# Performance work log

Hardware: AMD Instinct MI355X
Metric: run time of the kernel (lower is better)

Reference implementation:

```python
import jax, jax.numpy as jnp
import numpy as np

HIDDEN = 1024


def setup_inputs() -> dict:
    key = jax.random.key(0)
    ks = jax.random.split(key, 8)
    B, S, H = 64, 2048, HIDDEN
    scale = 1.0 / np.sqrt(H)
    return {
        "decoder_hidden": jax.random.normal(ks[0], (B, H), jnp.float32),
        "encoder_outputs": jax.random.normal(ks[1], (B, S, 2 * H), jnp.float32),
        "coverage": jax.random.uniform(ks[2], (B, S), jnp.float32),
        "mask": jnp.ones((B, S), jnp.int32),
        # parameters (nn.Linear weight layout: (out, in); we store transposed for x @ W)
        "W_h": jax.random.normal(ks[3], (2 * H, H), jnp.float32) * scale,
        "W_d": jax.random.normal(ks[4], (H, H), jnp.float32) * scale,
        "W_c": jax.random.normal(ks[5], (1, H), jnp.float32) * scale,
        "v": jax.random.normal(ks[6], (H, 1), jnp.float32) * scale,
    }


def reference(decoder_hidden, encoder_outputs, coverage, mask, W_h, W_d, W_c, v):
    # energy: (B, S, H) = tanh(enc@W_h + dec@W_d broadcast over S + coverage*W_c)
    enc_proj = jnp.einsum("bse,eh->bsh", encoder_outputs, W_h)
    dec_proj = (decoder_hidden @ W_d)[:, None, :]            # (B,1,H)
    cov_proj = coverage[:, :, None] * W_c[0][None, None, :]  # (B,S,H)
    energy = jnp.tanh(enc_proj + dec_proj + cov_proj)
    scores = jnp.einsum("bsh,h->bs", energy, v[:, 0])        # (B,S)
    scores = jnp.where(mask == 0, jnp.float32(-10000.0), scores)
    attn_weights = jax.nn.softmax(scores, axis=1)            # (B,S)
    coverage_new = coverage + attn_weights
    context = jnp.einsum("bs,bse->be", attn_weights, encoder_outputs)  # (B,2H)
    return (context, attn_weights, coverage_new)
```

## Files before the change

kernel.cpp:

```cpp
#include <hip/hip_runtime.h>
#include <hip/hip_bf16.h>
#include <stdint.h>

#define BATCH 64
#define SEQ   2048
#define HID   1024
#define EDIM  2048

#define BM 64
#define BK 32
#define KSTEPS (EDIM / BK)
#define SMEM_BYTES 141568

typedef __bf16 bf16x8 __attribute__((ext_vector_type(8)));
typedef float  f32x4  __attribute__((ext_vector_type(4)));

__device__ __forceinline__ unsigned short f2bf(float x) {
    __hip_bfloat16 h = __float2bfloat16(x);
    return __builtin_bit_cast(unsigned short, h);
}

__device__ __forceinline__ uint4 pack8(float4 f0, float4 f1) {
    uint4 r;
    r.x = (unsigned)f2bf(f0.x) | ((unsigned)f2bf(f0.y) << 16);
    r.y = (unsigned)f2bf(f0.z) | ((unsigned)f2bf(f0.w) << 16);
    r.z = (unsigned)f2bf(f1.x) | ((unsigned)f2bf(f1.y) << 16);
    r.w = (unsigned)f2bf(f1.z) | ((unsigned)f2bf(f1.w) << 16);
    return r;
}

__device__ __forceinline__ void gload16(const void* g, void* l) {
    __builtin_amdgcn_global_load_lds(
        (const __attribute__((address_space(1))) void*)g,
        (__attribute__((address_space(3))) void*)l, 16, 0, 0);
}

__global__ void wh_transpose_kernel(const float* __restrict__ Wh,
                                    unsigned short* __restrict__ Wt) {
    __shared__ float tile[32][33];
    int bx = blockIdx.x & 63;
    int by = blockIdx.x >> 6;
    int e0 = bx * 32, h0 = by * 32;
    int tx = threadIdx.x & 31, ty = threadIdx.x >> 5;
    #pragma unroll
    for (int i = 0; i < 4; ++i)
        tile[ty + 8 * i][tx] = Wh[(size_t)(e0 + ty + 8 * i) * HID + h0 + tx];
    __syncthreads();
    if (ty < 4) {
        uint4 wv;
        unsigned short* ws = (unsigned short*)&wv;
        #pragma unroll
        for (int j = 0; j < 8; ++j) ws[j] = f2bf(tile[ty * 8 + j][tx]);
        *(uint4*)&Wt[((size_t)(e0 >> 3) + ty) * 8192 + (size_t)(h0 + tx) * 8] = wv;
    }
}

__global__ void dec_proj_kernel(const float* __restrict__ dec,
                                const float* __restrict__ Wd,
                                float* __restrict__ dp) {
    int gid = blockIdx.x * 256 + threadIdx.x;
    int b = gid >> 10, h = gid & 1023;
    const float* dr = dec + b * HID;
    float acc = 0.f;
    #pragma unroll 4
    for (int k = 0; k < HID; ++k) acc = fmaf(dr[k], Wd[(size_t)k * HID + h], acc);
    dp[gid] = acc;
}

__global__ __launch_bounds__(1024, 4) void scores_kernel(
    const float* __restrict__ enc, const float* __restrict__ cov,
    const unsigned short* __restrict__ Wt, const float* __restrict__ dp,
    const float* __restrict__ Wc, const float* __restrict__ vv,
    float* __restrict__ scores)
{
    extern __shared__ char smem[];
    unsigned short* Blbase = (unsigned short*)smem;
    unsigned short* Albase = (unsigned short*)(smem + 131072);
    float* cov_s = (float*)(smem + 139264);
    float* sred  = (float*)(smem + 139520);

    const int tid  = threadIdx.x;
    const int lane = tid & 63;
    const int wid  = tid >> 6;
    const int wm   = wid >> 3;
    const int wn   = wid & 7;
    const int c15  = lane & 15;
    const int g    = lane >> 4;
    const int rsl  = (c15 & 3) ^ ((c15 >> 2) & 3);

    const int b  = blockIdx.x >> 5;
    const int s0 = (blockIdx.x & 31) * BM;

    const float* Abase = enc + (size_t)(b * SEQ + s0) * EDIM;

    const int arow = tid >> 2;
    const int ag   = tid & 3;
    const int asl  = ag ^ ((arow & 3) ^ ((arow >> 2) & 3));

    f32x4 acc[2][8];
    #pragma unroll
    for (int mi = 0; mi < 2; ++mi)
        #pragma unroll
        for (int nj = 0; nj < 8; ++nj)
            #pragma unroll
            for (int r = 0; r < 4; ++r) acc[mi][nj][r] = 0.f;

    if (tid < BM) cov_s[tid] = cov[b * SEQ + s0 + tid];

    {
        const unsigned short* bsrc = Wt + (size_t)tid * 8;
        unsigned short* bdst = Blbase + tid * 8;
        #pragma unroll
        for (int j = 0; j < 4; ++j)
            gload16(bsrc + (size_t)j * 8192, bdst + j * 8192);
        if (tid < 256) {
            const float* ap = Abase + (size_t)arow * EDIM + ag * 8;
            *(uint4*)(Albase + arow * 32 + asl * 8) =
                pack8(*(const float4*)ap, *(const float4*)(ap + 4));
        }
    }
    __syncthreads();

    float4 a0n, a1n;
    for (int kk = 0; kk < KSTEPS; ++kk) {
        const int cur = kk & 1, nxt = cur ^ 1;
        const unsigned short* Bcur = Blbase + cur * 32768;
        const unsigned short* Acur = Albase + cur * 2048;

        if (kk + 1 < KSTEPS) {
            const unsigned short* bsrc = Wt + (size_t)(kk + 1) * 32768 + (size_t)tid * 8;
            unsigned short* bdst = Blbase + nxt * 32768 + tid * 8;
            #pragma unroll
            for (int j = 0; j < 4; ++j)
                gload16(bsrc + (size_t)j * 8192, bdst + j * 8192);
            if (tid < 256) {
                const float* ap = Abase + (size_t)arow * EDIM + (kk + 1) * BK + ag * 8;
                a0n = *(const float4*)ap;
                a1n = *(const float4*)(ap + 4);
            }
        }

        bf16x8 afr0 = *(const bf16x8*)(Acur + (wm * 32 + c15) * 32 + ((g ^ rsl) * 8));
        bf16x8 afr1 = *(const bf16x8*)(Acur + (wm * 32 + 16 + c15) * 32 + ((g ^ rsl) * 8));
        #pragma unroll
        for (int nj = 0; nj < 8; ++nj) {
            bf16x8 bfr = *(const bf16x8*)(Bcur + ((size_t)(g * 1024 + wn * 128 + nj * 16 + c15)) * 8);
            acc[0][nj] = __builtin_amdgcn_mfma_f32_16x16x32_bf16(afr0, bfr, acc[0][nj], 0, 0, 0);
            acc[1][nj] = __builtin_amdgcn_mfma_f32_16x16x32_bf16(afr1, bfr, acc[1][nj], 0, 0, 0);
        }

        if (kk + 1 < KSTEPS && tid < 256)
            *(uint4*)(Albase + nxt * 2048 + arow * 32 + asl * 8) = pack8(a0n, a1n);
        __syncthreads();
    }

    float spart[2][4] = {{0.f,0.f,0.f,0.f},{0.f,0.f,0.f,0.f}};
    #pragma unroll
    for (int nj = 0; nj < 8; ++nj) {
        const int h = wn * 128 + nj * 16 + c15;
        const float dv  = dp[b * HID + h];
        const float wcv = Wc[h];
        const float vvv = vv[h];
        #pragma unroll
        for (int mi = 0; mi < 2; ++mi) {
            #pragma unroll
            for (int r = 0; r < 4; ++r) {
                const int row = wm * 32 + mi * 16 + g * 4 + r;
                float pre = acc[mi][nj][r] + dv + cov_s[row] * wcv;
                float pc = fminf(pre, 20.0f);
                float e2 = __expf(2.0f * pc);
                float th = (e2 - 1.0f) / (e2 + 1.0f);
                spart[mi][r] = fmaf(th, vvv, spart[mi][r]);
            }
        }
    }
    #pragma unroll
    for (int mi = 0; mi < 2; ++mi) {
        #pragma unroll
        for (int r = 0; r < 4; ++r) {
            float x = spart[mi][r];
            x += __shfl_xor(x, 1);
            x += __shfl_xor(x, 2);
            x += __shfl_xor(x, 4);
            x += __shfl_xor(x, 8);
            if (c15 == 0) sred[(wm * 32 + mi * 16 + g * 4 + r) * 8 + wn] = x;
        }
    }
    __syncthreads();
    if (tid < BM) {
        float s = 0.f;
        #pragma unroll
        for (int w = 0; w < 8; ++w) s += sred[tid * 8 + w];
        scores[b * SEQ + s0 + tid] = s;
    }
}

__global__ void softmax_kernel(const float* __restrict__ scores,
                               const int* __restrict__ mask,
                               const float* __restrict__ cov,
                               float* __restrict__ out)
{
    __shared__ float red[8];
    int b = blockIdx.x, tid = threadIdx.x;
    float vals[8];
    float mx = -1e30f;
    #pragma unroll
    for (int i = 0; i < 8; ++i) {
        int s = tid + i * 256;
        float sc = scores[b * SEQ + s];
        sc = (mask[b * SEQ + s] == 0) ? -10000.0f : sc;
        vals[i] = sc;
        mx = fmaxf(mx, sc);
    }
    for (int m = 1; m < 64; m <<= 1) mx = fmaxf(mx, __shfl_xor(mx, m));
    if ((tid & 63) == 0) red[tid >> 6] = mx;
    __syncthreads();
    mx = fmaxf(fmaxf(red[0], red[1]), fmaxf(red[2], red[3]));
    float sum = 0.f;
    #pragma unroll
    for (int i = 0; i < 8; ++i) { vals[i] = __expf(vals[i] - mx); sum += vals[i]; }
    for (int m = 1; m < 64; m <<= 1) sum += __shfl_xor(sum, m);
    if ((tid & 63) == 0) red[4 + (tid >> 6)] = sum;
    __syncthreads();
    sum = red[4] + red[5] + red[6] + red[7];
    float inv = 1.0f / sum;
    float* attn = out + BATCH * EDIM;
    float* covn = attn + BATCH * SEQ;
    #pragma unroll
    for (int i = 0; i < 8; ++i) {
        int s = tid + i * 256;
        float w = vals[i] * inv;
        attn[b * SEQ + s] = w;
        covn[b * SEQ + s] = cov[b * SEQ + s] + w;
    }
}

__global__ void context_kernel(const float* __restrict__ enc,
                               const float* __restrict__ attn,
                               float* __restrict__ ctx)
{
    __shared__ float w_s[SEQ];
    int b  = blockIdx.x >> 3;
    int e0 = (blockIdx.x & 7) * 256;
    int tid = threadIdx.x;
    for (int i = tid; i < SEQ; i += 256) w_s[i] = attn[b * SEQ + i];
    __syncthreads();
    const float* ep = enc + (size_t)b * SEQ * EDIM + e0 + tid;
    float acc = 0.f;
    #pragma unroll 8
    for (int s = 0; s < SEQ; ++s) acc = fmaf(w_s[s], ep[(size_t)s * EDIM], acc);
    ctx[b * EDIM + e0 + tid] = acc;
}

extern "C" void kernel_launch(void* const* d_in, const int* in_sizes, int n_in,
                              void* d_out, int out_size, void* d_ws, size_t ws_size,
                              hipStream_t stream) {
    const float* dec  = (const float*)d_in[0];
    const float* enc  = (const float*)d_in[1];
    const float* cov  = (const float*)d_in[2];
    const int*   mask = (const int*)d_in[3];
    const float* Wh   = (const float*)d_in[4];
    const float* Wd   = (const float*)d_in[5];
    const float* Wc   = (const float*)d_in[6];
    const float* v    = (const float*)d_in[7];
    float* out = (float*)d_out;

    unsigned short* Wt = (unsigned short*)d_ws;
    float* dp     = (float*)((char*)d_ws + (size_t)HID * EDIM * 2);
    float* scores = dp + BATCH * HID;

    (void)hipFuncSetAttribute((const void*)scores_kernel,
                              hipFuncAttributeMaxDynamicSharedMemorySize, SMEM_BYTES);

    wh_transpose_kernel<<<dim3(64 * 32), dim3(256), 0, stream>>>(Wh, Wt);
    dec_proj_kernel<<<dim3(BATCH * HID / 256), dim3(256), 0, stream>>>(dec, Wd, dp);
    scores_kernel<<<dim3(BATCH * (SEQ / BM)), dim3(1024), SMEM_BYTES, stream>>>(
        enc, cov, Wt, dp, Wc, v, scores);
    softmax_kernel<<<dim3(BATCH), dim3(256), 0, stream>>>(scores, mask, cov, out);
    context_kernel<<<dim3(BATCH * (EDIM / 256)), dim3(256), 0, stream>>>(enc, out + BATCH * EDIM, out);
}
```

Before: 1.072 ms.

## Switch scores GEMM to 32x32x16 MFMA with 8 waves per block

The scores kernel moves from 16x16x32 bf16 MFMA across 16 waves to 32x32x16 MFMA across 8 waves (512 threads). Each wave now covers all 64 rows and a 128-column slice. The A tile gets a new XOR swizzle, the B tile staging layout changes to match, and the epilogue reduction is reshaped for the 32-wide output layout. The aim is to halve LDS fragment traffic per block and use the larger, more efficient MFMA shape. The cost is fewer resident waves to hide global and LDS latency, and more accumulator registers per wave.

```diff
diff --git a/kernel.cpp b/kernel.cpp
--- a/kernel.cpp
+++ b/kernel.cpp
@@ -13,7 +13,7 @@
 #define SMEM_BYTES 141568
 
 typedef __bf16 bf16x8 __attribute__((ext_vector_type(8)));
-typedef float  f32x4  __attribute__((ext_vector_type(4)));
+typedef float  f32x16 __attribute__((ext_vector_type(16)));
 
 __device__ __forceinline__ unsigned short f2bf(float x) {
     __hip_bfloat16 h = __float2bfloat16(x);
@@ -33,6 +33,10 @@
     __builtin_amdgcn_global_load_lds(
         (const __attribute__((address_space(1))) void*)g,
         (__attribute__((address_space(3))) void*)l, 16, 0, 0);
+}
+
+__device__ __forceinline__ int a_addr(int row, int g) {
+    return ((row << 6) + (g << 4)) ^ ((row & 7) << 4);
 }
 
 __global__ void wh_transpose_kernel(const float* __restrict__ Wh,
@@ -67,26 +71,23 @@
     dp[gid] = acc;
 }
 
-__global__ __launch_bounds__(1024, 4) void scores_kernel(
+__global__ __launch_bounds__(512, 2) void scores_kernel(
     const float* __restrict__ enc, const float* __restrict__ cov,
     const unsigned short* __restrict__ Wt, const float* __restrict__ dp,
     const float* __restrict__ Wc, const float* __restrict__ vv,
     float* __restrict__ scores)
 {
     extern __shared__ char smem[];
-    unsigned short* Blbase = (unsigned short*)smem;
-    unsigned short* Albase = (unsigned short*)(smem + 131072);
+    unsigned short* BlS  = (unsigned short*)smem;
+    char*  AlB   = smem + 131072;
     float* cov_s = (float*)(smem + 139264);
     float* sred  = (float*)(smem + 139520);
 
     const int tid  = threadIdx.x;
     const int lane = tid & 63;
     const int wid  = tid >> 6;
-    const int wm   = wid >> 3;
-    const int wn   = wid & 7;
-    const int c15  = lane & 15;
-    const int g    = lane >> 4;
-    const int rsl  = (c15 & 3) ^ ((c15 >> 2) & 3);
+    const int l31  = lane & 31;
+    const int hi   = lane >> 5;
 
     const int b  = blockIdx.x >> 5;
     const int s0 = (blockIdx.x & 31) * BM;
@@ -95,27 +96,26 @@
 
     const int arow = tid >> 2;
     const int ag   = tid & 3;
-    const int asl  = ag ^ ((arow & 3) ^ ((arow >> 2) & 3));
-
-    f32x4 acc[2][8];
+
+    f32x16 acc[2][4];
     #pragma unroll
     for (int mi = 0; mi < 2; ++mi)
         #pragma unroll
-        for (int nj = 0; nj < 8; ++nj)
-            #pragma unroll
-            for (int r = 0; r < 4; ++r) acc[mi][nj][r] = 0.f;
+        for (int nj = 0; nj < 4; ++nj)
+            #pragma unroll
+            for (int r = 0; r < 16; ++r) acc[mi][nj][r] = 0.f;
 
     if (tid < BM) cov_s[tid] = cov[b * SEQ + s0 + tid];
 
     {
         const unsigned short* bsrc = Wt + (size_t)tid * 8;
-        unsigned short* bdst = Blbase + tid * 8;
-        #pragma unroll
-        for (int j = 0; j < 4; ++j)
-            gload16(bsrc + (size_t)j * 8192, bdst + j * 8192);
+        unsigned short* bdst = BlS + tid * 8;
+        #pragma unroll
+        for (int j = 0; j < 8; ++j)
+            gload16(bsrc + (size_t)j * 4096, bdst + j * 4096);
         if (tid < 256) {
             const float* ap = Abase + (size_t)arow * EDIM + ag * 8;
-            *(uint4*)(Albase + arow * 32 + asl * 8) =
+            *(uint4*)(AlB + a_addr(arow, ag)) =
                 pack8(*(const float4*)ap, *(const float4*)(ap + 4));
         }
     }
@@ -124,15 +124,15 @@
     float4 a0n, a1n;
     for (int kk = 0; kk < KSTEPS; ++kk) {
         const int cur = kk & 1, nxt = cur ^ 1;
-        const unsigned short* Bcur = Blbase + cur * 32768;
-        const unsigned short* Acur = Albase + cur * 2048;
+        const unsigned short* Bcur = BlS + cur * 32768;
+        const char* Acur = AlB + cur * 4096;
 
         if (kk + 1 < KSTEPS) {
             const unsigned short* bsrc = Wt + (size_t)(kk + 1) * 32768 + (size_t)tid * 8;
-            unsigned short* bdst = Blbase + nxt * 32768 + tid * 8;
-            #pragma unroll
-            for (int j = 0; j < 4; ++j)
-                gload16(bsrc + (size_t)j * 8192, bdst + j * 8192);
+            unsigned short* bdst = BlS + nxt * 32768 + tid * 8;
+            #pragma unroll
+            for (int j = 0; j < 8; ++j)
+                gload16(bsrc + (size_t)j * 4096, bdst + j * 4096);
             if (tid < 256) {
                 const float* ap = Abase + (size_t)arow * EDIM + (kk + 1) * BK + ag * 8;
                 a0n = *(const float4*)ap;
@@ -140,50 +140,55 @@
             }
         }
 
-        bf16x8 afr0 = *(const bf16x8*)(Acur + (wm * 32 + c15) * 32 + ((g ^ rsl) * 8));
-        bf16x8 afr1 = *(const bf16x8*)(Acur + (wm * 32 + 16 + c15) * 32 + ((g ^ rsl) * 8));
-        #pragma unroll
-        for (int nj = 0; nj < 8; ++nj) {
-            bf16x8 bfr = *(const bf16x8*)(Bcur + ((size_t)(g * 1024 + wn * 128 + nj * 16 + c15)) * 8);
-            acc[0][nj] = __builtin_amdgcn_mfma_f32_16x16x32_bf16(afr0, bfr, acc[0][nj], 0, 0, 0);
-            acc[1][nj] = __builtin_amdgcn_mfma_f32_16x16x32_bf16(afr1, bfr, acc[1][nj], 0, 0, 0);
+        #pragma unroll
+        for (int ks = 0; ks < 2; ++ks) {
+            const int g = 2 * ks + hi;
+            bf16x8 afr0 = *(const bf16x8*)(Acur + a_addr(l31, g));
+            bf16x8 afr1 = *(const bf16x8*)(Acur + a_addr(32 + l31, g));
+            #pragma unroll
+            for (int nj = 0; nj < 4; ++nj) {
+                bf16x8 bfr = *(const bf16x8*)(Bcur +
+                    ((size_t)g * 8192 + (size_t)(wid * 128 + nj * 32 + l31) * 8));
+                acc[0][nj] = __builtin_amdgcn_mfma_f32_32x32x16_bf16(
+                    afr0, bfr, acc[0][nj], 0, 0, 0);
+                acc[1][nj] = __builtin_amdgcn_mfma_f32_32x32x16_bf16(
+                    afr1, bfr, acc[1][nj], 0, 0, 0);
+            }
         }
 
         if (kk + 1 < KSTEPS && tid < 256)
-            *(uint4*)(Albase + nxt * 2048 + arow * 32 + asl * 8) = pack8(a0n, a1n);
+            *(uint4*)(AlB + nxt * 4096 + a_addr(arow, ag)) = pack8(a0n, a1n);
         __syncthreads();
     }
 
-    float spart[2][4] = {{0.f,0.f,0.f,0.f},{0.f,0.f,0.f,0.f}};
-    #pragma unroll
-    for (int nj = 0; nj < 8; ++nj) {
-        const int h = wn * 128 + nj * 16 + c15;
-        const float dv  = dp[b * HID + h];
-        const float wcv = Wc[h];
-        const float vvv = vv[h];
-        #pragma unroll
-        for (int mi = 0; mi < 2; ++mi) {
-            #pragma unroll
-            for (int r = 0; r < 4; ++r) {
-                const int row = wm * 32 + mi * 16 + g * 4 + r;
-                float pre = acc[mi][nj][r] + dv + cov_s[row] * wcv;
+    float dv[4], wcv[4], vvv[4];
+    #pragma unroll
+    for (int nj = 0; nj < 4; ++nj) {
+        const int h = wid * 128 + nj * 32 + l31;
+        dv[nj]  = dp[b * HID + h];
+        wcv[nj] = Wc[h];
+        vvv[nj] = vv[h];
+    }
+    #pragma unroll
+    for (int mi = 0; mi < 2; ++mi) {
+        #pragma unroll
+        for (int r = 0; r < 16; ++r) {
+            const int row = mi * 32 + (r & 3) + 8 * (r >> 2) + 4 * hi;
+            const float cv = cov_s[row];
+            float x = 0.f;
+            #pragma unroll
+            for (int nj = 0; nj < 4; ++nj) {
+                float pre = acc[mi][nj][r] + dv[nj] + cv * wcv[nj];
                 float pc = fminf(pre, 20.0f);
                 float e2 = __expf(2.0f * pc);
-                float th = (e2 - 1.0f) / (e2 + 1.0f);
-                spart[mi][r] = fmaf(th, vvv, spart[mi][r]);
+                x = fmaf((e2 - 1.0f) / (e2 + 1.0f), vvv[nj], x);
             }
-        }
-    }
-    #pragma unroll
-    for (int mi = 0; mi < 2; ++mi) {
-        #pragma unroll
-        for (int r = 0; r < 4; ++r) {
-            float x = spart[mi][r];
             x += __shfl_xor(x, 1);
             x += __shfl_xor(x, 2);
             x += __shfl_xor(x, 4);
             x += __shfl_xor(x, 8);
-            if (c15 == 0) sred[(wm * 32 + mi * 16 + g * 4 + r) * 8 + wn] = x;
+            x += __shfl_xor(x, 16);
+            if (l31 == 0) sred[row * 8 + wid] = x;
         }
     }
     __syncthreads();
@@ -274,7 +279,7 @@
 
     wh_transpose_kernel<<<dim3(64 * 32), dim3(256), 0, stream>>>(Wh, Wt);
     dec_proj_kernel<<<dim3(BATCH * HID / 256), dim3(256), 0, stream>>>(dec, Wd, dp);
-    scores_kernel<<<dim3(BATCH * (SEQ / BM)), dim3(1024), SMEM_BYTES, stream>>>(
+    scores_kernel<<<dim3(BATCH * (SEQ / BM)), dim3(512), SMEM_BYTES, stream>>>(
         enc, cov, Wt, dp, Wc, v, scores);
     softmax_kernel<<<dim3(BATCH), dim3(256), 0, stream>>>(scores, mask, cov, out);
     context_kernel<<<dim3(BATCH * (EDIM / 256)), dim3(256), 0, stream>>>(enc, out + BATCH * EDIM, out);
```

Result: slower. 1.159 ms (+8.2%).

## Split scores GEMM across two N-halves and split context over sequence chunks

Applied to the files above, without the earlier changes.

The scores kernel now uses 512-thread blocks that each compute half of the hidden dimension, which halves LDS per block so more blocks can be resident. The two partial score vectors are summed inside softmax. The context reduction is split into four sequence chunks with a separate reduce kernel, giving more blocks for parallelism, and encoder reads use nontemporal loads. The cost is that the encoder tile is read and converted twice in the scores kernel, plus an extra kernel launch and a partial-sum buffer.

```diff
diff --git a/kernel.cpp b/kernel.cpp
--- a/kernel.cpp
+++ b/kernel.cpp
@@ -8,19 +8,21 @@
 #define EDIM  2048
 
 #define BM 64
+#define BN 512
 #define BK 32
 #define KSTEPS (EDIM / BK)
-#define SMEM_BYTES 141568
+#define BS (BATCH * SEQ)
+#define SMEM_BYTES 76032
 
 typedef __bf16 bf16x8 __attribute__((ext_vector_type(8)));
-typedef float  f32x4  __attribute__((ext_vector_type(4)));
+typedef float  f32x4a __attribute__((ext_vector_type(4)));
 
 __device__ __forceinline__ unsigned short f2bf(float x) {
     __hip_bfloat16 h = __float2bfloat16(x);
     return __builtin_bit_cast(unsigned short, h);
 }
 
-__device__ __forceinline__ uint4 pack8(float4 f0, float4 f1) {
+__device__ __forceinline__ uint4 pack8(f32x4a f0, f32x4a f1) {
     uint4 r;
     r.x = (unsigned)f2bf(f0.x) | ((unsigned)f2bf(f0.y) << 16);
     r.y = (unsigned)f2bf(f0.z) | ((unsigned)f2bf(f0.w) << 16);
@@ -33,6 +35,15 @@
     __builtin_amdgcn_global_load_lds(
         (const __attribute__((address_space(1))) void*)g,
         (__attribute__((address_space(3))) void*)l, 16, 0, 0);
+}
+
+__device__ __forceinline__ f32x4a ntload4(const float* p) {
+    return __builtin_nontemporal_load((const f32x4a*)p);
+}
+
+__device__ __forceinline__ int a_addr(int row, int g) {
+    int slot = g ^ ((row & 3) ^ ((row >> 2) & 3));
+    return (row << 6) + (slot << 4);
 }
 
 __global__ void wh_transpose_kernel(const float* __restrict__ Wh,
@@ -51,7 +62,7 @@
         unsigned short* ws = (unsigned short*)&wv;
         #pragma unroll
         for (int j = 0; j < 8; ++j) ws[j] = f2bf(tile[ty * 8 + j][tx]);
-        *(uint4*)&Wt[((size_t)(e0 >> 3) + ty) * 8192 + (size_t)(h0 + tx) * 8] = wv;
+        *(uint4*)&Wt[(size_t)((e0 >> 3) + ty) * 8192 + (size_t)(h0 + tx) * 8] = wv;
     }
 }
 
@@ -67,37 +78,41 @@
     dp[gid] = acc;
 }
 
-__global__ __launch_bounds__(1024, 4) void scores_kernel(
+#define MFMA16(a, bfv, c) __builtin_amdgcn_mfma_f32_16x16x32_bf16(a, bfv, c, 0, 0, 0)
+
+__global__ __launch_bounds__(512, 4) void scores_kernel(
     const float* __restrict__ enc, const float* __restrict__ cov,
     const unsigned short* __restrict__ Wt, const float* __restrict__ dp,
     const float* __restrict__ Wc, const float* __restrict__ vv,
-    float* __restrict__ scores)
+    float* __restrict__ spart_out)
 {
     extern __shared__ char smem[];
-    unsigned short* Blbase = (unsigned short*)smem;
-    unsigned short* Albase = (unsigned short*)(smem + 131072);
-    float* cov_s = (float*)(smem + 139264);
-    float* sred  = (float*)(smem + 139520);
+    unsigned short* BlS = (unsigned short*)smem;
+    char*  AlB   = smem + 65536;
+    float* cov_s = (float*)(smem + 73728);
+    float* sred  = (float*)(smem + 73984);
 
     const int tid  = threadIdx.x;
     const int lane = tid & 63;
     const int wid  = tid >> 6;
-    const int wm   = wid >> 3;
-    const int wn   = wid & 7;
+    const int wm   = wid >> 2;
+    const int wn   = wid & 3;
     const int c15  = lane & 15;
-    const int g    = lane >> 4;
-    const int rsl  = (c15 & 3) ^ ((c15 >> 2) & 3);
-
-    const int b  = blockIdx.x >> 5;
-    const int s0 = (blockIdx.x & 31) * BM;
+    const int g4   = lane >> 4;
+
+    const int bid  = blockIdx.x;
+    const int half = bid & 1;
+    const int m    = bid >> 1;
+    const int b    = m >> 5;
+    const int s0   = (m & 31) * BM;
 
     const float* Abase = enc + (size_t)(b * SEQ + s0) * EDIM;
-
     const int arow = tid >> 2;
     const int ag   = tid & 3;
-    const int asl  = ag ^ ((arow & 3) ^ ((arow >> 2) & 3));
-
-    f32x4 acc[2][8];
+
+    const unsigned short* Bsrc = Wt + half * 4096 + (size_t)tid * 8;
+
+    f32x4a acc[2][8];
     #pragma unroll
     for (int mi = 0; mi < 2; ++mi)
         #pragma unroll
@@ -108,56 +123,53 @@
     if (tid < BM) cov_s[tid] = cov[b * SEQ + s0 + tid];
 
     {
-        const unsigned short* bsrc = Wt + (size_t)tid * 8;
-        unsigned short* bdst = Blbase + tid * 8;
         #pragma unroll
         for (int j = 0; j < 4; ++j)
-            gload16(bsrc + (size_t)j * 8192, bdst + j * 8192);
+            gload16(Bsrc + (size_t)j * 8192, BlS + j * 4096 + tid * 8);
         if (tid < 256) {
             const float* ap = Abase + (size_t)arow * EDIM + ag * 8;
-            *(uint4*)(Albase + arow * 32 + asl * 8) =
-                pack8(*(const float4*)ap, *(const float4*)(ap + 4));
-        }
-    }
-    __syncthreads();
-
-    float4 a0n, a1n;
+            *(uint4*)(AlB + a_addr(arow, ag)) = pack8(ntload4(ap), ntload4(ap + 4));
+        }
+    }
+    __syncthreads();
+
     for (int kk = 0; kk < KSTEPS; ++kk) {
         const int cur = kk & 1, nxt = cur ^ 1;
-        const unsigned short* Bcur = Blbase + cur * 32768;
-        const unsigned short* Acur = Albase + cur * 2048;
+        const unsigned short* Bcur = BlS + cur * 16384;
+        const char* Acur = AlB + cur * 4096;
+        f32x4a a0n, a1n;
 
         if (kk + 1 < KSTEPS) {
-            const unsigned short* bsrc = Wt + (size_t)(kk + 1) * 32768 + (size_t)tid * 8;
-            unsigned short* bdst = Blbase + nxt * 32768 + tid * 8;
+            const unsigned short* bs = Bsrc + (size_t)(kk + 1) * 32768;
+            unsigned short* bd = BlS + nxt * 16384 + tid * 8;
             #pragma unroll
             for (int j = 0; j < 4; ++j)
-                gload16(bsrc + (size_t)j * 8192, bdst + j * 8192);
+                gload16(bs + (size_t)j * 8192, bd + j * 4096);
             if (tid < 256) {
                 const float* ap = Abase + (size_t)arow * EDIM + (kk + 1) * BK + ag * 8;
-                a0n = *(const float4*)ap;
-                a1n = *(const float4*)(ap + 4);
+                a0n = ntload4(ap); a1n = ntload4(ap + 4);
             }
         }
 
-        bf16x8 afr0 = *(const bf16x8*)(Acur + (wm * 32 + c15) * 32 + ((g ^ rsl) * 8));
-        bf16x8 afr1 = *(const bf16x8*)(Acur + (wm * 32 + 16 + c15) * 32 + ((g ^ rsl) * 8));
+        bf16x8 afr0 = *(const bf16x8*)(Acur + a_addr(wm * 32 + c15, g4));
+        bf16x8 afr1 = *(const bf16x8*)(Acur + a_addr(wm * 32 + 16 + c15, g4));
         #pragma unroll
         for (int nj = 0; nj < 8; ++nj) {
-            bf16x8 bfr = *(const bf16x8*)(Bcur + ((size_t)(g * 1024 + wn * 128 + nj * 16 + c15)) * 8);
-            acc[0][nj] = __builtin_amdgcn_mfma_f32_16x16x32_bf16(afr0, bfr, acc[0][nj], 0, 0, 0);
-            acc[1][nj] = __builtin_amdgcn_mfma_f32_16x16x32_bf16(afr1, bfr, acc[1][nj], 0, 0, 0);
+            bf16x8 bfr = *(const bf16x8*)(Bcur + (size_t)g4 * 4096 +
+                                          (size_t)(wn * 128 + nj * 16 + c15) * 8);
+            acc[0][nj] = MFMA16(afr0, bfr, acc[0][nj]);
+            acc[1][nj] = MFMA16(afr1, bfr, acc[1][nj]);
         }
 
         if (kk + 1 < KSTEPS && tid < 256)
-            *(uint4*)(Albase + nxt * 2048 + arow * 32 + asl * 8) = pack8(a0n, a1n);
+            *(uint4*)(AlB + nxt * 4096 + a_addr(arow, ag)) = pack8(a0n, a1n);
         __syncthreads();
     }
 
     float spart[2][4] = {{0.f,0.f,0.f,0.f},{0.f,0.f,0.f,0.f}};
     #pragma unroll
     for (int nj = 0; nj < 8; ++nj) {
-        const int h = wn * 128 + nj * 16 + c15;
+        const int h = half * BN + wn * 128 + nj * 16 + c15;
         const float dv  = dp[b * HID + h];
         const float wcv = Wc[h];
         const float vvv = vv[h];
@@ -165,12 +177,11 @@
         for (int mi = 0; mi < 2; ++mi) {
             #pragma unroll
             for (int r = 0; r < 4; ++r) {
-                const int row = wm * 32 + mi * 16 + g * 4 + r;
+                const int row = wm * 32 + mi * 16 + g4 * 4 + r;
                 float pre = acc[mi][nj][r] + dv + cov_s[row] * wcv;
                 float pc = fminf(pre, 20.0f);
                 float e2 = __expf(2.0f * pc);
-                float th = (e2 - 1.0f) / (e2 + 1.0f);
-                spart[mi][r] = fmaf(th, vvv, spart[mi][r]);
+                spart[mi][r] = fmaf((e2 - 1.0f) / (e2 + 1.0f), vvv, spart[mi][r]);
             }
         }
     }
@@ -183,19 +194,17 @@
             x += __shfl_xor(x, 2);
             x += __shfl_xor(x, 4);
             x += __shfl_xor(x, 8);
-            if (c15 == 0) sred[(wm * 32 + mi * 16 + g * 4 + r) * 8 + wn] = x;
+            if (c15 == 0) sred[(wm * 32 + mi * 16 + g4 * 4 + r) * 4 + wn] = x;
         }
     }
     __syncthreads();
     if (tid < BM) {
-        float s = 0.f;
-        #pragma unroll
-        for (int w = 0; w < 8; ++w) s += sred[tid * 8 + w];
-        scores[b * SEQ + s0 + tid] = s;
-    }
-}
-
-__global__ void softmax_kernel(const float* __restrict__ scores,
+        float s = sred[tid * 4] + sred[tid * 4 + 1] + sred[tid * 4 + 2] + sred[tid * 4 + 3];
+        spart_out[(size_t)half * BS + b * SEQ + s0 + tid] = s;
+    }
+}
+
+__global__ void softmax_kernel(const float* __restrict__ spart,
                                const int* __restrict__ mask,
                                const float* __restrict__ cov,
                                float* __restrict__ out)
@@ -207,7 +216,7 @@
     #pragma unroll
     for (int i = 0; i < 8; ++i) {
         int s = tid + i * 256;
-        float sc = scores[b * SEQ + s];
+        float sc = spart[b * SEQ + s] + spart[BS + b * SEQ + s];
         sc = (mask[b * SEQ + s] == 0) ? -10000.0f : sc;
         vals[i] = sc;
         mx = fmaxf(mx, sc);
@@ -235,21 +244,33 @@
     }
 }
 
-__global__ void context_kernel(const float* __restrict__ enc,
-                               const float* __restrict__ attn,
-                               float* __restrict__ ctx)
+__global__ void context_partial_kernel(const float* __restrict__ enc,
+                                       const float* __restrict__ attn,
+                                       float* __restrict__ cpart)
 {
-    __shared__ float w_s[SEQ];
-    int b  = blockIdx.x >> 3;
-    int e0 = (blockIdx.x & 7) * 256;
+    __shared__ float w_s[512];
+    int bid = blockIdx.x;
+    int sc = bid & 3;
+    int e0 = ((bid >> 2) & 7) * 256;
+    int b  = bid >> 5;
     int tid = threadIdx.x;
-    for (int i = tid; i < SEQ; i += 256) w_s[i] = attn[b * SEQ + i];
-    __syncthreads();
-    const float* ep = enc + (size_t)b * SEQ * EDIM + e0 + tid;
+    w_s[tid] = attn[b * SEQ + sc * 512 + tid];
+    w_s[tid + 256] = attn[b * SEQ + sc * 512 + 256 + tid];
+    __syncthreads();
+    const float* ep = enc + ((size_t)b * SEQ + sc * 512) * EDIM + e0 + tid;
     float acc = 0.f;
     #pragma unroll 8
-    for (int s = 0; s < SEQ; ++s) acc = fmaf(w_s[s], ep[(size_t)s * EDIM], acc);
-    ctx[b * EDIM + e0 + tid] = acc;
+    for (int s = 0; s < 512; ++s)
+        acc = fmaf(w_s[s], __builtin_nontemporal_load(ep + (size_t)s * EDIM), acc);
+    cpart[((size_t)sc * BATCH + b) * EDIM + e0 + tid] = acc;
+}
+
+__global__ void ctx_reduce_kernel(const float* __restrict__ cpart,
+                                  float* __restrict__ ctx)
+{
+    int idx = blockIdx.x * 256 + threadIdx.x;
+    ctx[idx] = cpart[idx] + cpart[BATCH * EDIM + idx] +
+               cpart[2 * BATCH * EDIM + idx] + cpart[3 * BATCH * EDIM + idx];
 }
 
 extern "C" void kernel_launch(void* const* d_in, const int* in_sizes, int n_in,
@@ -266,16 +287,19 @@
     float* out = (float*)d_out;
 
     unsigned short* Wt = (unsigned short*)d_ws;
-    float* dp     = (float*)((char*)d_ws + (size_t)HID * EDIM * 2);
-    float* scores = dp + BATCH * HID;
+    float* dp    = (float*)((char*)d_ws + (size_t)HID * EDIM * 2);
+    float* spart = dp + BATCH * HID;
+    float* cpart = spart + 2 * BS;
 
     (void)hipFuncSetAttribute((const void*)scores_kernel,
                               hipFuncAttributeMaxDynamicSharedMemorySize, SMEM_BYTES);
 
     wh_transpose_kernel<<<dim3(64 * 32), dim3(256), 0, stream>>>(Wh, Wt);
     dec_proj_kernel<<<dim3(BATCH * HID / 256), dim3(256), 0, stream>>>(dec, Wd, dp);
-    scores_kernel<<<dim3(BATCH * (SEQ / BM)), dim3(1024), SMEM_BYTES, stream>>>(
-        enc, cov, Wt, dp, Wc, v, scores);
-    softmax_kernel<<<dim3(BATCH), dim3(256), 0, stream>>>(scores, mask, cov, out);
-    context_kernel<<<dim3(BATCH * (EDIM / 256)), dim3(256), 0, stream>>>(enc, out + BATCH * EDIM, out);
-}
+    scores_kernel<<<dim3((BS / BM) * 2), dim3(512), SMEM_BYTES, stream>>>(
+        enc, cov, Wt, dp, Wc, v, spart);
+    softmax_kernel<<<dim3(BATCH), dim3(256), 0, stream>>>(spart, mask, cov, out);
+    context_partial_kernel<<<dim3(BATCH * 8 * 4), dim3(256), 0, stream>>>(
+        enc, out + BATCH * EDIM, cpart);
+    ctx_reduce_kernel<<<dim3(BATCH * EDIM / 256), dim3(256), 0, stream>>>(cpart, out);
+}
```

Result: no change. 1.063 ms (-0.8%).
